# Optimization experiments

Hardware: AMD Instinct MI355X
Metric: run time of the kernel (lower is better)

The kernel has to match this reference:

```python
import jax, jax.numpy as jnp
import numpy as np

N, E = 50000, 1600000
F_IN, EDGE_DIM, HID, HEADS, NCLS = 64, 16, 128, 4, 40
C = HID // HEADS  # per-head dim = 32


def setup_inputs() -> dict:
    key = jax.random.key(0)
    ks = jax.random.split(key, 20)
    s = 0.1
    inp = {
        'x': jax.random.normal(ks[0], (N, F_IN), jnp.float32),
        'edge_index': jax.random.randint(ks[1], (2, E), 0, N, jnp.int64),
        'edge_attr': jax.random.normal(ks[2], (E, EDGE_DIM), jnp.float32),
        # layer 1 params
        'W1': jax.random.normal(ks[3], (HID, F_IN), jnp.float32) * s,
        'as1': jax.random.normal(ks[4], (HEADS, C), jnp.float32) * s,
        'ad1': jax.random.normal(ks[5], (HEADS, C), jnp.float32) * s,
        'ae1': jax.random.normal(ks[6], (HEADS, C), jnp.float32) * s,
        'We1': jax.random.normal(ks[7], (HID, EDGE_DIM), jnp.float32) * s,
        'b1': jnp.zeros((HID,), jnp.float32),
        # layer 2 params
        'W2': jax.random.normal(ks[8], (HID, HID), jnp.float32) * s,
        'as2': jax.random.normal(ks[9], (HEADS, C), jnp.float32) * s,
        'ad2': jax.random.normal(ks[10], (HEADS, C), jnp.float32) * s,
        'ae2': jax.random.normal(ks[11], (HEADS, C), jnp.float32) * s,
        'We2': jax.random.normal(ks[12], (HID, EDGE_DIM), jnp.float32) * s,
        'b2': jnp.zeros((HID,), jnp.float32),
        # final classifier
        'Wlin': jax.random.normal(ks[13], (NCLS, HID), jnp.float32) * s,
        'blin': jnp.zeros((NCLS,), jnp.float32),
    }
    return inp


def gat_conv(x, src, dst, eattr, W, a_s, a_d, a_e, We, b):
    """PyG GATConv (concat=True, add_self_loops=True, fill_value='mean'), eval mode."""
    n = x.shape[0]
    H, Cd = a_s.shape
    h = (x @ W.T).reshape(n, H, Cd)  # [N,H,C]
    # self-loop edge_attr = per-destination mean of incoming edge_attr
    cnt = jax.ops.segment_sum(jnp.ones((dst.shape[0],), eattr.dtype), dst, num_segments=n)
    mean_ea = jax.ops.segment_sum(eattr, dst, num_segments=n) / jnp.maximum(cnt, 1.0)[:, None]
    loops = jnp.arange(n, dtype=src.dtype)
    s_idx = jnp.concatenate([src, loops])
    d_idx = jnp.concatenate([dst, loops])
    ea = jnp.concatenate([eattr, mean_ea], axis=0)  # [E+N, edge_dim]
    e = (ea @ We.T).reshape(-1, H, Cd)
    # edge-wise attention logits
    alpha = (h * a_s).sum(-1)[s_idx] + (h * a_d).sum(-1)[d_idx] + (e * a_e).sum(-1)  # [E+N,H]
    alpha = jax.nn.leaky_relu(alpha, 0.2)
    # segment softmax over destination neighborhoods (every node has a self-loop)
    amax = jax.ops.segment_max(alpha, d_idx, num_segments=n)
    ex = jnp.exp(alpha - amax[d_idx])
    den = jax.ops.segment_sum(ex, d_idx, num_segments=n)
    coef = ex / (den[d_idx] + 1e-16)
    out = jax.ops.segment_sum(h[s_idx] * coef[:, :, None], d_idx, num_segments=n)
    return out.reshape(n, H * Cd) + b


def reference(x, edge_index, edge_attr, W1, as1, ad1, ae1, We1, b1,
              W2, as2, ad2, ae2, We2, b2, Wlin, blin):
    src, dst = edge_index[0], edge_index[1]
    h = jax.nn.relu(gat_conv(x, src, dst, edge_attr, W1, as1, ad1, ae1, We1, b1))
    h = jax.nn.relu(gat_conv(h, src, dst, edge_attr, W2, as2, ad2, ae2, We2, b2))
    logits = h @ Wlin.T + blin
    return jax.nn.log_softmax(logits, axis=1)
```

## Files before the change

kernel.cpp:

```cpp
#include <hip/hip_runtime.h>
#include <hip/hip_bf16.h>
#include <math.h>


#define CHUNK 2048

typedef __attribute__((ext_vector_type(8))) short short8;
typedef __attribute__((ext_vector_type(4))) float floatx4;

__device__ __forceinline__ unsigned short f2bf(float f) {
  unsigned u = __float_as_uint(f);
  unsigned r = u + 0x7FFFu + ((u >> 16) & 1u);
  return (unsigned short)(r >> 16);
}
__device__ __forceinline__ float bf2f(unsigned short b) {
  return __uint_as_float(((unsigned)b) << 16);
}

__global__ __launch_bounds__(128) void wa_kernel(const float* __restrict__ ae1,
                                                 const float* __restrict__ We1,
                                                 const float* __restrict__ ae2,
                                                 const float* __restrict__ We2,
                                                 float* __restrict__ Wa) {
  int t = threadIdx.x;
  const float* ae = (t < 64) ? ae1 : ae2;
  const float* We = (t < 64) ? We1 : We2;
  int h = (t >> 4) & 3;
  int d = t & 15;
  float s = 0.f;
  for (int c = 0; c < 32; ++c) s += ae[h * 32 + c] * We[(h * 32 + c) * 16 + d];
  Wa[t] = s;
}

__global__ __launch_bounds__(256) void alphaseq_kernel(const float* __restrict__ ea,
                                                       const float* __restrict__ Wa,
                                                       uint2* __restrict__ tA1,
                                                       uint2* __restrict__ tA2, int E) {
  __shared__ float wa[128];
  if (threadIdx.x < 128) wa[threadIdx.x] = Wa[threadIdx.x];
  __syncthreads();
  int e = blockIdx.x * 256 + threadIdx.x;
  if (e >= E) return;
  const float4* p = (const float4*)(ea + (size_t)e * 16);
  float4 q0 = p[0], q1 = p[1], q2 = p[2], q3 = p[3];
  float v[16] = {q0.x, q0.y, q0.z, q0.w, q1.x, q1.y, q1.z, q1.w,
                 q2.x, q2.y, q2.z, q2.w, q3.x, q3.y, q3.z, q3.w};
  unsigned short rr[8];
#pragma unroll
  for (int h = 0; h < 8; ++h) {
    float s = 0.f;
#pragma unroll
    for (int d = 0; d < 16; ++d) s += v[d] * wa[h * 16 + d];
    rr[h] = f2bf(s);
  }
  uint2 lo, hi;
  lo.x = ((unsigned)rr[1] << 16) | rr[0];
  lo.y = ((unsigned)rr[3] << 16) | rr[2];
  hi.x = ((unsigned)rr[5] << 16) | rr[4];
  hi.y = ((unsigned)rr[7] << 16) | rr[6];
  tA1[e] = lo;
  tA2[e] = hi;
}

__global__ __launch_bounds__(512) void hist_kernel(const int* __restrict__ dst,
                                                   int* __restrict__ bucketCnt,
                                                   int E, int NB) {
  __shared__ int hist[512];
  const int tid = threadIdx.x;
  hist[tid] = 0;
  __syncthreads();
  const int e0 = blockIdx.x * CHUNK, e1 = min(e0 + CHUNK, E);
  for (int e = e0 + tid; e < e1; e += 512) atomicAdd(&hist[dst[e] >> 7], 1);
  __syncthreads();
  if (tid < NB && hist[tid]) atomicAdd(&bucketCnt[tid], hist[tid]);
}

__global__ __launch_bounds__(512) void scanB_kernel(const int* __restrict__ bucketCnt,
                                                    int* __restrict__ bucketOffs,
                                                    int* __restrict__ bucketPos,
                                                    int* __restrict__ offs,
                                                    int NB, int N, int E) {
  __shared__ int sc[512];
  const int tid = threadIdx.x;
  const int v = (tid < NB) ? bucketCnt[tid] : 0;
  sc[tid] = v;
  __syncthreads();
  for (int off = 1; off < 512; off <<= 1) {
    int t = (tid >= off) ? sc[tid - off] : 0;
    __syncthreads();
    sc[tid] += t;
    __syncthreads();
  }
  const int excl = sc[tid] - v;
  if (tid < NB) { bucketOffs[tid] = excl; bucketPos[tid] = excl; }
  if (tid == 0) { bucketOffs[NB] = E; offs[N] = E; }
}

__global__ __launch_bounds__(512) void partB_kernel(const int* __restrict__ src,
                                                    const int* __restrict__ dst,
                                                    const uint2* __restrict__ tA1,
                                                    const uint2* __restrict__ tA2,
                                                    int* __restrict__ bucketPos,
                                                    int4* __restrict__ binned16,
                                                    int* __restrict__ binned4,
                                                    int E, int NB) {
  __shared__ int hist[512], sc[512], lbase[513], gbase[512], lcnt[512];
  __shared__ int4 stg16[CHUNK];
  __shared__ int stg4[CHUNK];
  const int tid = threadIdx.x;
  const int e0 = blockIdx.x * CHUNK;
  const int e1 = min(e0 + CHUNK, E);
  hist[tid] = 0; lcnt[tid] = 0;
  __syncthreads();
  for (int e = e0 + tid; e < e1; e += 512) atomicAdd(&hist[dst[e] >> 7], 1);
  __syncthreads();
  sc[tid] = hist[tid];
  __syncthreads();
  for (int off = 1; off < 512; off <<= 1) {
    int t = (tid >= off) ? sc[tid - off] : 0;
    __syncthreads();
    sc[tid] += t;
    __syncthreads();
  }
  lbase[tid + 1] = sc[tid];
  if (tid == 0) lbase[0] = 0;
  if (tid < NB && hist[tid] > 0) gbase[tid] = atomicAdd(&bucketPos[tid], hist[tid]);
  __syncthreads();
  for (int e = e0 + tid; e < e1; e += 512) {
    const int d = dst[e];
    const int b = d >> 7;
    const int lr = atomicAdd(&lcnt[b], 1);
    const uint2 a1 = tA1[e];
    const uint2 a2 = tA2[e];
    int4 v;
    v.x = (src[e] & 0xFFFF) | ((d & 127) << 16);
    v.y = (int)a1.x;
    v.z = (int)a1.y;
    v.w = (int)a2.x;
    const int sp = lbase[b] + lr;
    stg16[sp] = v;
    stg4[sp] = (int)a2.y;
  }
  __syncthreads();
  const int total = e1 - e0;
  for (int t = tid; t < total; t += 512) {
    int lo = 0, hi = 511;
    while (lo < hi) {
      int mid = (lo + hi + 1) >> 1;
      if (lbase[mid] <= t) lo = mid; else hi = mid - 1;
    }
    const int g = gbase[lo] + (t - lbase[lo]);
    binned16[g] = stg16[t];
    binned4[g] = stg4[t];
  }
}

__global__ __launch_bounds__(256) void passC_kernel(const int4* __restrict__ binned16,
                                                    const int* __restrict__ binned4,
                                                    const int* __restrict__ bucketOffs,
                                                    int* __restrict__ srcS,
                                                    uint2* __restrict__ aeS1,
                                                    uint2* __restrict__ aeS2,
                                                    int* __restrict__ offs, int N) {
  __shared__ int cnt[128], dbase[129], dpos[128];
  const int tid = threadIdx.x;
  const int b = blockIdx.x;
  const int bo = bucketOffs[b], be = bucketOffs[b + 1];
  const int m = be - bo;
  if (tid < 128) { cnt[tid] = 0; dpos[tid] = 0; }
  __syncthreads();
  for (int t = tid; t < m; t += 256) {
    const int4 v = binned16[bo + t];
    atomicAdd(&cnt[(v.x >> 16) & 127], 1);
  }
  __syncthreads();
  for (int off = 1; off < 128; off <<= 1) {
    int t = (tid < 128 && tid >= (unsigned)off) ? cnt[tid - off] : 0;
    __syncthreads();
    if (tid < 128) cnt[tid] += t;
    __syncthreads();
  }
  if (tid == 0) dbase[0] = 0;
  if (tid < 128) dbase[tid + 1] = cnt[tid];
  __syncthreads();
  const int dcnt = min(128, N - (b << 7));
  if (tid < dcnt) offs[(b << 7) + tid] = bo + dbase[tid];
  for (int t = tid; t < m; t += 256) {
    const int4 v = binned16[bo + t];
    const int w4 = binned4[bo + t];
    const int dl = (v.x >> 16) & 127;
    const int p = dbase[dl] + atomicAdd(&dpos[dl], 1);
    srcS[bo + p] = v.x & 0xFFFF;
    aeS1[bo + p] = make_uint2((unsigned)v.y, (unsigned)v.z);
    aeS2[bo + p] = make_uint2((unsigned)v.w, (unsigned)w4);
  }
}

__global__ __launch_bounds__(256) void cvt3_kernel(const float* __restrict__ a,
                                                   unsigned short* __restrict__ ao, int na,
                                                   const float* __restrict__ b,
                                                   unsigned short* __restrict__ bo, int nb,
                                                   const float* __restrict__ c,
                                                   unsigned short* __restrict__ co, int nc) {
  int i = blockIdx.x * 256 + threadIdx.x;
  if (i < na) ao[i] = f2bf(a[i]);
  else if (i < na + nb) bo[i - na] = f2bf(b[i - na]);
  else if (i < na + nb + nc) co[i - na - nb] = f2bf(c[i - na - nb]);
}

__global__ __launch_bounds__(256) void cvtw_kernel(const float* __restrict__ Wlin,
                                                   unsigned short* __restrict__ whi,
                                                   unsigned short* __restrict__ wlo) {
  int i = blockIdx.x * 256 + threadIdx.x;
  if (i >= 48 * 128) return;
  float v = (i < 40 * 128) ? Wlin[i] : 0.f;
  unsigned short h = f2bf(v);
  whi[i] = h;
  wlo[i] = f2bf(v - bf2f(h));
}

__global__ __launch_bounds__(256) void gemm_mfma_kernel(const unsigned short* __restrict__ X,
                                                        const unsigned short* __restrict__ Wb,
                                                        unsigned short* __restrict__ H,
                                                        int n, int K) {
  const int w = threadIdx.x >> 6;
  const int lane = threadIdx.x & 63;
  const int m0 = blockIdx.x * 64;
  const int quad = lane >> 4;
  const int l15 = lane & 15;
  floatx4 acc[4][2];
#pragma unroll
  for (int mt = 0; mt < 4; ++mt)
#pragma unroll
    for (int nt = 0; nt < 2; ++nt) acc[mt][nt] = (floatx4)(0.f);

  int rowm[4];
#pragma unroll
  for (int mt = 0; mt < 4; ++mt) {
    int r = m0 + mt * 16 + l15;
    rowm[mt] = (r < n) ? r : (n - 1);
  }
  const int ncol0 = (w << 5) + l15;

  for (int kc = 0; kc < K; kc += 32) {
    const int koff = kc + (quad << 3);
    short8 a[4], b[2];
#pragma unroll
    for (int mt = 0; mt < 4; ++mt)
      a[mt] = *(const short8*)(X + (size_t)rowm[mt] * K + koff);
#pragma unroll
    for (int nt = 0; nt < 2; ++nt)
      b[nt] = *(const short8*)(Wb + (size_t)(ncol0 + nt * 16) * K + koff);
#pragma unroll
    for (int mt = 0; mt < 4; ++mt)
#pragma unroll
      for (int nt = 0; nt < 2; ++nt)
        acc[mt][nt] = __builtin_amdgcn_mfma_f32_16x16x32_bf16(a[mt], b[nt], acc[mt][nt], 0, 0, 0);
  }
#pragma unroll
  for (int mt = 0; mt < 4; ++mt) {
    const int rbase = m0 + mt * 16 + (quad << 2);
#pragma unroll
    for (int nt = 0; nt < 2; ++nt) {
      const int col = ncol0 + nt * 16;
#pragma unroll
      for (int r = 0; r < 4; ++r) {
        const int row = rbase + r;
        if (row < n) H[(size_t)row * 128 + col] = f2bf(acc[mt][nt][r]);
      }
    }
  }
}

__global__ __launch_bounds__(256) void score_kernel(const unsigned short* __restrict__ h,
                                                    const float* __restrict__ a_s,
                                                    const float* __restrict__ a_d,
                                                    float* __restrict__ ssc,
                                                    float* __restrict__ dsc, int n) {
  int gid = blockIdx.x * 256 + threadIdx.x;
  int node = gid >> 6;
  int lane = threadIdx.x & 63;
  if (node >= n) return;
  int ch = lane * 2;
  ushort2 hq = *(const ushort2*)(h + (size_t)node * 128 + ch);
  float h0 = bf2f(hq.x), h1 = bf2f(hq.y);
  float ps = h0 * a_s[ch] + h1 * a_s[ch + 1];
  float pd = h0 * a_d[ch] + h1 * a_d[ch + 1];
#pragma unroll
  for (int off = 8; off; off >>= 1) {
    ps += __shfl_xor(ps, off, 16);
    pd += __shfl_xor(pd, off, 16);
  }
  if ((lane & 15) == 0) {
    int head = lane >> 4;
    ssc[node * 4 + head] = ps;
    dsc[node * 4 + head] = pd;
  }
}

__device__ __forceinline__ float leaky02(float a) { return a > 0.f ? a : 0.2f * a; }
__device__ __forceinline__ float sel4(float4 v, int h) {
  return (h == 0) ? v.x : (h == 1) ? v.y : (h == 2) ? v.z : v.w;
}

__global__ __launch_bounds__(256) void agg_kernel(const unsigned short* __restrict__ hin,
                                                  const float* __restrict__ ssc,
                                                  const float* __restrict__ dsc,
                                                  const unsigned short* __restrict__ aeS,
                                                  const int* __restrict__ offs,
                                                  const int* __restrict__ srcS,
                                                  const float* __restrict__ bias,
                                                  unsigned short* __restrict__ hout, int n) {
  __shared__ int sbuf[4][64];
  __shared__ float pbuf[4][256];
  const int tid = threadIdx.x;
  const int wv = tid >> 6;
  const int lane = tid & 63;
  const int node = blockIdx.x * 4 + wv;
  if (node >= n) return;
  const int l32 = lane & 31;
  const int half = lane >> 5;
  const int ch4 = l32 * 4;
  const int headB = l32 >> 3;
  const float4 dv = *(const float4*)(dsc + (size_t)node * 4);
  float4 l4 = make_float4(0.f, 0.f, 0.f, 0.f);
  float4 sa = make_float4(0.f, 0.f, 0.f, 0.f);
  float acc[4] = {0.f, 0.f, 0.f, 0.f};
  const int j0 = offs[node], j1 = offs[node + 1];

  for (int jc = j0; jc < j1; jc += 64) {
    const int len = min(64, j1 - jc);
    float4 p4 = make_float4(0.f, 0.f, 0.f, 0.f);
    int sv = 0;
    if (lane < len) {
      const int j = jc + lane;
      sv = srcS[j];
      const ushort4 aq = *(const ushort4*)(aeS + (size_t)j * 4);
      const float4 ae4 = make_float4(bf2f(aq.x), bf2f(aq.y), bf2f(aq.z), bf2f(aq.w));
      const float4 ss4 = *(const float4*)(ssc + (size_t)sv * 4);
      sa.x += ae4.x; sa.y += ae4.y; sa.z += ae4.z; sa.w += ae4.w;
      p4.x = __expf(leaky02(ss4.x + dv.x + ae4.x));
      p4.y = __expf(leaky02(ss4.y + dv.y + ae4.y));
      p4.z = __expf(leaky02(ss4.z + dv.z + ae4.z));
      p4.w = __expf(leaky02(ss4.w + dv.w + ae4.w));
    }
    sbuf[wv][lane] = sv;
    *(float4*)(&pbuf[wv][lane * 4]) = p4;
    l4.x += p4.x; l4.y += p4.y; l4.z += p4.z; l4.w += p4.w;
    int k = 0;
    for (; k + 8 <= len; k += 8) {
      int kk0 = k + half, kk1 = k + 2 + half, kk2 = k + 4 + half, kk3 = k + 6 + half;
      int s0 = sbuf[wv][kk0], s1 = sbuf[wv][kk1], s2 = sbuf[wv][kk2], s3 = sbuf[wv][kk3];
      float p0 = pbuf[wv][kk0 * 4 + headB], p1 = pbuf[wv][kk1 * 4 + headB];
      float p2 = pbuf[wv][kk2 * 4 + headB], p3 = pbuf[wv][kk3 * 4 + headB];
      uint2 d0 = *(const uint2*)(hin + (size_t)s0 * 128 + ch4);
      uint2 d1 = *(const uint2*)(hin + (size_t)s1 * 128 + ch4);
      uint2 d2 = *(const uint2*)(hin + (size_t)s2 * 128 + ch4);
      uint2 d3 = *(const uint2*)(hin + (size_t)s3 * 128 + ch4);
      acc[0] += p0 * __uint_as_float(d0.x << 16);
      acc[1] += p0 * __uint_as_float(d0.x & 0xFFFF0000u);
      acc[2] += p0 * __uint_as_float(d0.y << 16);
      acc[3] += p0 * __uint_as_float(d0.y & 0xFFFF0000u);
      acc[0] += p1 * __uint_as_float(d1.x << 16);
      acc[1] += p1 * __uint_as_float(d1.x & 0xFFFF0000u);
      acc[2] += p1 * __uint_as_float(d1.y << 16);
      acc[3] += p1 * __uint_as_float(d1.y & 0xFFFF0000u);
      acc[0] += p2 * __uint_as_float(d2.x << 16);
      acc[1] += p2 * __uint_as_float(d2.x & 0xFFFF0000u);
      acc[2] += p2 * __uint_as_float(d2.y << 16);
      acc[3] += p2 * __uint_as_float(d2.y & 0xFFFF0000u);
      acc[0] += p3 * __uint_as_float(d3.x << 16);
      acc[1] += p3 * __uint_as_float(d3.x & 0xFFFF0000u);
      acc[2] += p3 * __uint_as_float(d3.y << 16);
      acc[3] += p3 * __uint_as_float(d3.y & 0xFFFF0000u);
    }
    for (; k < len; k += 2) {
      int kk = k + half;
      if (kk < len) {
        int s = sbuf[wv][kk];
        float p = pbuf[wv][kk * 4 + headB];
        uint2 d = *(const uint2*)(hin + (size_t)s * 128 + ch4);
        acc[0] += p * __uint_as_float(d.x << 16);
        acc[1] += p * __uint_as_float(d.x & 0xFFFF0000u);
        acc[2] += p * __uint_as_float(d.y << 16);
        acc[3] += p * __uint_as_float(d.y & 0xFFFF0000u);
      }
    }
  }

#pragma unroll
  for (int off = 32; off; off >>= 1) {
    sa.x += __shfl_xor(sa.x, off);
    sa.y += __shfl_xor(sa.y, off);
    sa.z += __shfl_xor(sa.z, off);
    sa.w += __shfl_xor(sa.w, off);
    l4.x += __shfl_xor(l4.x, off);
    l4.y += __shfl_xor(l4.y, off);
    l4.z += __shfl_xor(l4.z, off);
    l4.w += __shfl_xor(l4.w, off);
  }
#pragma unroll
  for (int i = 0; i < 4; ++i) acc[i] += __shfl_xor(acc[i], 32);

  const int deg = j1 - j0;
  const float invd = 1.f / fmaxf((float)deg, 1.f);
  const float ssn = ssc[(size_t)node * 4 + headB];
  const float aloop = leaky02(ssn + sel4(dv, headB) + sel4(sa, headB) * invd);
  const float pl = __expf(aloop);
  const float lF = sel4(l4, headB) + pl;
  const uint2 hd = *(const uint2*)(hin + (size_t)node * 128 + ch4);
  const float hv0 = __uint_as_float(hd.x << 16);
  const float hv1 = __uint_as_float(hd.x & 0xFFFF0000u);
  const float hv2 = __uint_as_float(hd.y << 16);
  const float hv3 = __uint_as_float(hd.y & 0xFFFF0000u);
  const float inv = 1.f / (lF + 1e-16f);
  const float4 bi = *(const float4*)(bias + ch4);
  const float o0 = fmaxf((acc[0] + pl * hv0) * inv + bi.x, 0.f);
  const float o1 = fmaxf((acc[1] + pl * hv1) * inv + bi.y, 0.f);
  const float o2 = fmaxf((acc[2] + pl * hv2) * inv + bi.z, 0.f);
  const float o3 = fmaxf((acc[3] + pl * hv3) * inv + bi.w, 0.f);
  if (half == 0) {
    ushort4 o;
    o.x = f2bf(o0); o.y = f2bf(o1); o.z = f2bf(o2); o.w = f2bf(o3);
    *(ushort4*)(hout + (size_t)node * 128 + ch4) = o;
  }
}

__global__ __launch_bounds__(256) void classifier_kernel(const unsigned short* __restrict__ h,
                                                         const unsigned short* __restrict__ Whi,
                                                         const unsigned short* __restrict__ Wlo,
                                                         const float* __restrict__ blin,
                                                         float* __restrict__ out, int n) {
  const int w = threadIdx.x >> 6;
  const int lane = threadIdx.x & 63;
  const int quad = lane >> 4;
  const int l15 = lane & 15;
  const int row0 = blockIdx.x * 64 + w * 16;
  if (row0 >= n) return;
  int rowm = row0 + l15;
  if (rowm >= n) rowm = n - 1;
  floatx4 acc[3];
#pragma unroll
  for (int nt = 0; nt < 3; ++nt) acc[nt] = (floatx4)(0.f);
  const size_t hbase = (size_t)rowm * 128;
#pragma unroll
  for (int kc = 0; kc < 128; kc += 32) {
    const int koff = kc + (quad << 3);
    short8 a = *(const short8*)(h + hbase + koff);
#pragma unroll
    for (int nt = 0; nt < 3; ++nt) {
      short8 bh = *(const short8*)(Whi + (size_t)(nt * 16 + l15) * 128 + koff);
      short8 bl = *(const short8*)(Wlo + (size_t)(nt * 16 + l15) * 128 + koff);
      acc[nt] = __builtin_amdgcn_mfma_f32_16x16x32_bf16(a, bh, acc[nt], 0, 0, 0);
      acc[nt] = __builtin_amdgcn_mfma_f32_16x16x32_bf16(a, bl, acc[nt], 0, 0, 0);
    }
  }
  const float bl0 = blin[l15];
  const float bl1 = blin[16 + l15];
  const float bl2 = (l15 < 8) ? blin[32 + l15] : 0.f;
#pragma unroll
  for (int r = 0; r < 4; ++r) {
    const int rrow = row0 + (quad << 2) + r;
    const float v0 = acc[0][r] + bl0;
    const float v1 = acc[1][r] + bl1;
    const float v2 = (l15 < 8) ? (acc[2][r] + bl2) : -INFINITY;
    float m = fmaxf(v0, fmaxf(v1, v2));
#pragma unroll
    for (int off = 8; off; off >>= 1) m = fmaxf(m, __shfl_xor(m, off, 16));
    const float e2 = (l15 < 8) ? __expf(v2 - m) : 0.f;
    float s = __expf(v0 - m) + __expf(v1 - m) + e2;
#pragma unroll
    for (int off = 8; off; off >>= 1) s += __shfl_xor(s, off, 16);
    const float ls = m + __logf(s);
    if (rrow < n) {
      float* po = out + (size_t)rrow * 40;
      po[l15] = v0 - ls;
      po[16 + l15] = v1 - ls;
      if (l15 < 8) po[32 + l15] = v2 - ls;
    }
  }
}

extern "C" void kernel_launch(void* const* d_in, const int* in_sizes, int n_in,
                              void* d_out, int out_size, void* d_ws, size_t ws_size,
                              hipStream_t stream) {
  const float* x    = (const float*)d_in[0];
  const int*   eidx = (const int*)d_in[1];
  const float* ea   = (const float*)d_in[2];
  const float* W1   = (const float*)d_in[3];
  const float* as1  = (const float*)d_in[4];
  const float* ad1  = (const float*)d_in[5];
  const float* ae1w = (const float*)d_in[6];
  const float* We1  = (const float*)d_in[7];
  const float* b1   = (const float*)d_in[8];
  const float* W2   = (const float*)d_in[9];
  const float* as2  = (const float*)d_in[10];
  const float* ad2  = (const float*)d_in[11];
  const float* ae2w = (const float*)d_in[12];
  const float* We2  = (const float*)d_in[13];
  const float* b2   = (const float*)d_in[14];
  const float* Wlin = (const float*)d_in[15];
  const float* blin = (const float*)d_in[16];
  float* out = (float*)d_out;

  const int N = in_sizes[0] / 64;
  const int E = in_sizes[1] / 2;
  const int* src = eidx;
  const int* dst = eidx + E;
  const int NB = (N + 127) >> 7;

  char* wsb = (char*)d_ws;
  size_t off = 0;
  auto alloc = [&](size_t bytes) -> void* {
    void* p = wsb + off;
    off = (off + bytes + 255) & ~(size_t)255;
    return p;
  };
  int* bucketCnt  = (int*)alloc(512 * 4);
  int* bucketOffs = (int*)alloc(513 * 4);
  int* bucketPos  = (int*)alloc(512 * 4);
  int* offs       = (int*)alloc((size_t)(N + 1) * 4);
  uint2* tA1      = (uint2*)alloc((size_t)E * 8);
  uint2* tA2      = (uint2*)alloc((size_t)E * 8);
  void* regC      = alloc((size_t)E * 16);
  int4* binned16  = (int4*)regC;
  unsigned short* hA = (unsigned short*)regC;
  void* regD      = alloc((size_t)E * 4);
  int* binned4    = (int*)regD;
  unsigned short* xb = (unsigned short*)regD;
  int* srcS       = (int*)alloc((size_t)E * 4);
  float* Wa       = (float*)alloc(128 * 4);
  unsigned short* Wb1 = (unsigned short*)alloc(128 * 64 * 2);
  unsigned short* Wb2 = (unsigned short*)alloc(128 * 128 * 2);
  unsigned short* Wlh = (unsigned short*)alloc(48 * 128 * 2);
  unsigned short* Wll = (unsigned short*)alloc(48 * 128 * 2);
  float* ssc      = (float*)alloc((size_t)N * 4 * 4);
  float* dsc      = (float*)alloc((size_t)N * 4 * 4);
  unsigned short* hB = (unsigned short*)alloc((size_t)N * 128 * 2);
  uint2* aeS1 = tA1;
  uint2* aeS2 = tA2;

  const int ge = (E + 255) / 256;
  const int gg = (N + 63) / 64;
  const int gs = (N + 3) / 4;
  const int gp = (E + CHUNK - 1) / CHUNK;
  const int ncvt = N * 64 + 128 * 64 + 128 * 128;

  hipMemsetAsync(bucketCnt, 0, 512 * 4, stream);
  wa_kernel<<<1, 128, 0, stream>>>(ae1w, We1, ae2w, We2, Wa);
  alphaseq_kernel<<<ge, 256, 0, stream>>>(ea, Wa, tA1, tA2, E);
  hist_kernel<<<gp, 512, 0, stream>>>(dst, bucketCnt, E, NB);
  scanB_kernel<<<1, 512, 0, stream>>>(bucketCnt, bucketOffs, bucketPos, offs, NB, N, E);
  partB_kernel<<<gp, 512, 0, stream>>>(src, dst, tA1, tA2, bucketPos, binned16, binned4, E, NB);
  passC_kernel<<<NB, 256, 0, stream>>>(binned16, binned4, bucketOffs, srcS, aeS1, aeS2, offs, N);

  cvt3_kernel<<<(ncvt + 255) / 256, 256, 0, stream>>>(x, xb, N * 64, W1, Wb1, 128 * 64,
                                                      W2, Wb2, 128 * 128);
  cvtw_kernel<<<24, 256, 0, stream>>>(Wlin, Wlh, Wll);

  gemm_mfma_kernel<<<gg, 256, 0, stream>>>(xb, Wb1, hA, N, 64);
  score_kernel<<<gs, 256, 0, stream>>>(hA, as1, ad1, ssc, dsc, N);
  agg_kernel<<<gs, 256, 0, stream>>>(hA, ssc, dsc, (const unsigned short*)aeS1, offs, srcS, b1, hB, N);

  gemm_mfma_kernel<<<gg, 256, 0, stream>>>(hB, Wb2, hA, N, 128);
  score_kernel<<<gs, 256, 0, stream>>>(hA, as2, ad2, ssc, dsc, N);
  agg_kernel<<<gs, 256, 0, stream>>>(hA, ssc, dsc, (const unsigned short*)aeS2, offs, srcS, b2, hB, N);

  classifier_kernel<<<gg, 256, 0, stream>>>(hB, Wlh, Wll, blin, out, N);
}
```

Baseline: 490.6 us.

## Fuse x bf16 conversion into first GEMM, add byte dest-local array, pack agg FMAs

The first-layer GEMM now reads fp32 x directly and converts to bf16 in registers. This removes the separate conversion pass over N*64 elements and its intermediate buffer. partB also writes a one-byte destination-local index per edge, so passC's histogram pass reads 1 byte instead of 16 per edge, at the cost of an extra write. The aggregation inner loop is restructured to use float2 vector accumulators, which may map to packed FMA instructions.

```diff
diff --git a/kernel.cpp b/kernel.cpp
--- a/kernel.cpp
+++ b/kernel.cpp
@@ -7,6 +7,7 @@
 
 typedef __attribute__((ext_vector_type(8))) short short8;
 typedef __attribute__((ext_vector_type(4))) float floatx4;
+typedef __attribute__((ext_vector_type(2))) float floatx2;
 
 __device__ __forceinline__ unsigned short f2bf(float f) {
   unsigned u = __float_as_uint(f);
@@ -103,10 +104,12 @@
                                                     int* __restrict__ bucketPos,
                                                     int4* __restrict__ binned16,
                                                     int* __restrict__ binned4,
+                                                    unsigned char* __restrict__ dlArr,
                                                     int E, int NB) {
   __shared__ int hist[512], sc[512], lbase[513], gbase[512], lcnt[512];
   __shared__ int4 stg16[CHUNK];
   __shared__ int stg4[CHUNK];
+  __shared__ unsigned char stg1[CHUNK];
   const int tid = threadIdx.x;
   const int e0 = blockIdx.x * CHUNK;
   const int e1 = min(e0 + CHUNK, E);
@@ -140,6 +143,7 @@
     const int sp = lbase[b] + lr;
     stg16[sp] = v;
     stg4[sp] = (int)a2.y;
+    stg1[sp] = (unsigned char)(d & 127);
   }
   __syncthreads();
   const int total = e1 - e0;
@@ -152,11 +156,13 @@
     const int g = gbase[lo] + (t - lbase[lo]);
     binned16[g] = stg16[t];
     binned4[g] = stg4[t];
+    dlArr[g] = stg1[t];
   }
 }
 
 __global__ __launch_bounds__(256) void passC_kernel(const int4* __restrict__ binned16,
                                                     const int* __restrict__ binned4,
+                                                    const unsigned char* __restrict__ dlArr,
                                                     const int* __restrict__ bucketOffs,
                                                     int* __restrict__ srcS,
                                                     uint2* __restrict__ aeS1,
@@ -169,10 +175,7 @@
   const int m = be - bo;
   if (tid < 128) { cnt[tid] = 0; dpos[tid] = 0; }
   __syncthreads();
-  for (int t = tid; t < m; t += 256) {
-    const int4 v = binned16[bo + t];
-    atomicAdd(&cnt[(v.x >> 16) & 127], 1);
-  }
+  for (int t = tid; t < m; t += 256) atomicAdd(&cnt[dlArr[bo + t]], 1);
   __syncthreads();
   for (int off = 1; off < 128; off <<= 1) {
     int t = (tid < 128 && tid >= (unsigned)off) ? cnt[tid - off] : 0;
@@ -196,16 +199,13 @@
   }
 }
 
-__global__ __launch_bounds__(256) void cvt3_kernel(const float* __restrict__ a,
+__global__ __launch_bounds__(256) void cvt2_kernel(const float* __restrict__ a,
                                                    unsigned short* __restrict__ ao, int na,
                                                    const float* __restrict__ b,
-                                                   unsigned short* __restrict__ bo, int nb,
-                                                   const float* __restrict__ c,
-                                                   unsigned short* __restrict__ co, int nc) {
+                                                   unsigned short* __restrict__ bo, int nb) {
   int i = blockIdx.x * 256 + threadIdx.x;
   if (i < na) ao[i] = f2bf(a[i]);
   else if (i < na + nb) bo[i - na] = f2bf(b[i - na]);
-  else if (i < na + nb + nc) co[i - na - nb] = f2bf(c[i - na - nb]);
 }
 
 __global__ __launch_bounds__(256) void cvtw_kernel(const float* __restrict__ Wlin,
@@ -217,6 +217,67 @@
   unsigned short h = f2bf(v);
   whi[i] = h;
   wlo[i] = f2bf(v - bf2f(h));
+}
+
+__global__ __launch_bounds__(256) void gemm_mfma_f32_kernel(const float* __restrict__ X,
+                                                            const unsigned short* __restrict__ Wb,
+                                                            unsigned short* __restrict__ H,
+                                                            int n) {
+  const int w = threadIdx.x >> 6;
+  const int lane = threadIdx.x & 63;
+  const int m0 = blockIdx.x * 64;
+  const int quad = lane >> 4;
+  const int l15 = lane & 15;
+  floatx4 acc[4][2];
+#pragma unroll
+  for (int mt = 0; mt < 4; ++mt)
+#pragma unroll
+    for (int nt = 0; nt < 2; ++nt) acc[mt][nt] = (floatx4)(0.f);
+
+  int rowm[4];
+#pragma unroll
+  for (int mt = 0; mt < 4; ++mt) {
+    int r = m0 + mt * 16 + l15;
+    rowm[mt] = (r < n) ? r : (n - 1);
+  }
+  const int ncol0 = (w << 5) + l15;
+
+#pragma unroll
+  for (int kc = 0; kc < 64; kc += 32) {
+    const int koff = kc + (quad << 3);
+    short8 a[4], b[2];
+#pragma unroll
+    for (int mt = 0; mt < 4; ++mt) {
+      const float* pr = X + (size_t)rowm[mt] * 64 + koff;
+      float4 q0 = *(const float4*)pr;
+      float4 q1 = *(const float4*)(pr + 4);
+      a[mt][0] = (short)f2bf(q0.x); a[mt][1] = (short)f2bf(q0.y);
+      a[mt][2] = (short)f2bf(q0.z); a[mt][3] = (short)f2bf(q0.w);
+      a[mt][4] = (short)f2bf(q1.x); a[mt][5] = (short)f2bf(q1.y);
+      a[mt][6] = (short)f2bf(q1.z); a[mt][7] = (short)f2bf(q1.w);
+    }
+#pragma unroll
+    for (int nt = 0; nt < 2; ++nt)
+      b[nt] = *(const short8*)(Wb + (size_t)(ncol0 + nt * 16) * 64 + koff);
+#pragma unroll
+    for (int mt = 0; mt < 4; ++mt)
+#pragma unroll
+      for (int nt = 0; nt < 2; ++nt)
+        acc[mt][nt] = __builtin_amdgcn_mfma_f32_16x16x32_bf16(a[mt], b[nt], acc[mt][nt], 0, 0, 0);
+  }
+#pragma unroll
+  for (int mt = 0; mt < 4; ++mt) {
+    const int rbase = m0 + mt * 16 + (quad << 2);
+#pragma unroll
+    for (int nt = 0; nt < 2; ++nt) {
+      const int col = ncol0 + nt * 16;
+#pragma unroll
+      for (int r = 0; r < 4; ++r) {
+        const int row = rbase + r;
+        if (row < n) H[(size_t)row * 128 + col] = f2bf(acc[mt][nt][r]);
+      }
+    }
+  }
 }
 
 __global__ __launch_bounds__(256) void gemm_mfma_kernel(const unsigned short* __restrict__ X,
@@ -325,7 +386,8 @@
   const float4 dv = *(const float4*)(dsc + (size_t)node * 4);
   float4 l4 = make_float4(0.f, 0.f, 0.f, 0.f);
   float4 sa = make_float4(0.f, 0.f, 0.f, 0.f);
-  float acc[4] = {0.f, 0.f, 0.f, 0.f};
+  floatx2 acc01 = (floatx2)(0.f);
+  floatx2 acc23 = (floatx2)(0.f);
   const int j0 = offs[node], j1 = offs[node + 1];
 
   for (int jc = j0; jc < j1; jc += 64) {
@@ -349,30 +411,29 @@
     l4.x += p4.x; l4.y += p4.y; l4.z += p4.z; l4.w += p4.w;
     int k = 0;
     for (; k + 8 <= len; k += 8) {
-      int kk0 = k + half, kk1 = k + 2 + half, kk2 = k + 4 + half, kk3 = k + 6 + half;
-      int s0 = sbuf[wv][kk0], s1 = sbuf[wv][kk1], s2 = sbuf[wv][kk2], s3 = sbuf[wv][kk3];
-      float p0 = pbuf[wv][kk0 * 4 + headB], p1 = pbuf[wv][kk1 * 4 + headB];
-      float p2 = pbuf[wv][kk2 * 4 + headB], p3 = pbuf[wv][kk3 * 4 + headB];
-      uint2 d0 = *(const uint2*)(hin + (size_t)s0 * 128 + ch4);
-      uint2 d1 = *(const uint2*)(hin + (size_t)s1 * 128 + ch4);
-      uint2 d2 = *(const uint2*)(hin + (size_t)s2 * 128 + ch4);
-      uint2 d3 = *(const uint2*)(hin + (size_t)s3 * 128 + ch4);
-      acc[0] += p0 * __uint_as_float(d0.x << 16);
-      acc[1] += p0 * __uint_as_float(d0.x & 0xFFFF0000u);
-      acc[2] += p0 * __uint_as_float(d0.y << 16);
-      acc[3] += p0 * __uint_as_float(d0.y & 0xFFFF0000u);
-      acc[0] += p1 * __uint_as_float(d1.x << 16);
-      acc[1] += p1 * __uint_as_float(d1.x & 0xFFFF0000u);
-      acc[2] += p1 * __uint_as_float(d1.y << 16);
-      acc[3] += p1 * __uint_as_float(d1.y & 0xFFFF0000u);
-      acc[0] += p2 * __uint_as_float(d2.x << 16);
-      acc[1] += p2 * __uint_as_float(d2.x & 0xFFFF0000u);
-      acc[2] += p2 * __uint_as_float(d2.y << 16);
-      acc[3] += p2 * __uint_as_float(d2.y & 0xFFFF0000u);
-      acc[0] += p3 * __uint_as_float(d3.x << 16);
-      acc[1] += p3 * __uint_as_float(d3.x & 0xFFFF0000u);
-      acc[2] += p3 * __uint_as_float(d3.y << 16);
-      acc[3] += p3 * __uint_as_float(d3.y & 0xFFFF0000u);
+      int s[4];
+      float p[4];
+      uint2 d[4];
+#pragma unroll
+      for (int u = 0; u < 4; ++u) {
+        const int kk = k + 2 * u + half;
+        s[u] = sbuf[wv][kk];
+        p[u] = pbuf[wv][kk * 4 + headB];
+      }
+#pragma unroll
+      for (int u = 0; u < 4; ++u)
+        d[u] = *(const uint2*)(hin + (size_t)s[u] * 128 + ch4);
+#pragma unroll
+      for (int u = 0; u < 4; ++u) {
+        floatx2 p2; p2.x = p[u]; p2.y = p[u];
+        floatx2 h01, h23;
+        h01.x = __uint_as_float(d[u].x << 16);
+        h01.y = __uint_as_float(d[u].x & 0xFFFF0000u);
+        h23.x = __uint_as_float(d[u].y << 16);
+        h23.y = __uint_as_float(d[u].y & 0xFFFF0000u);
+        acc01 += p2 * h01;
+        acc23 += p2 * h23;
+      }
     }
     for (; k < len; k += 2) {
       int kk = k + half;
@@ -380,14 +441,19 @@
         int s = sbuf[wv][kk];
         float p = pbuf[wv][kk * 4 + headB];
         uint2 d = *(const uint2*)(hin + (size_t)s * 128 + ch4);
-        acc[0] += p * __uint_as_float(d.x << 16);
-        acc[1] += p * __uint_as_float(d.x & 0xFFFF0000u);
-        acc[2] += p * __uint_as_float(d.y << 16);
-        acc[3] += p * __uint_as_float(d.y & 0xFFFF0000u);
+        floatx2 p2; p2.x = p; p2.y = p;
+        floatx2 h01, h23;
+        h01.x = __uint_as_float(d.x << 16);
+        h01.y = __uint_as_float(d.x & 0xFFFF0000u);
+        h23.x = __uint_as_float(d.y << 16);
+        h23.y = __uint_as_float(d.y & 0xFFFF0000u);
+        acc01 += p2 * h01;
+        acc23 += p2 * h23;
       }
     }
   }
 
+  float acc[4] = {acc01.x, acc01.y, acc23.x, acc23.y};
 #pragma unroll
   for (int off = 32; off; off >>= 1) {
     sa.x += __shfl_xor(sa.x, off);
@@ -525,9 +591,8 @@
   void* regC      = alloc((size_t)E * 16);
   int4* binned16  = (int4*)regC;
   unsigned short* hA = (unsigned short*)regC;
-  void* regD      = alloc((size_t)E * 4);
-  int* binned4    = (int*)regD;
-  unsigned short* xb = (unsigned short*)regD;
+  int* binned4    = (int*)alloc((size_t)E * 4);
+  unsigned char* dlArr = (unsigned char*)alloc((size_t)E);
   int* srcS       = (int*)alloc((size_t)E * 4);
   float* Wa       = (float*)alloc(128 * 4);
   unsigned short* Wb1 = (unsigned short*)alloc(128 * 64 * 2);
@@ -544,21 +609,22 @@
   const int gg = (N + 63) / 64;
   const int gs = (N + 3) / 4;
   const int gp = (E + CHUNK - 1) / CHUNK;
-  const int ncvt = N * 64 + 128 * 64 + 128 * 128;
+  const int ncvt = 128 * 64 + 128 * 128;
 
   hipMemsetAsync(bucketCnt, 0, 512 * 4, stream);
   wa_kernel<<<1, 128, 0, stream>>>(ae1w, We1, ae2w, We2, Wa);
   alphaseq_kernel<<<ge, 256, 0, stream>>>(ea, Wa, tA1, tA2, E);
   hist_kernel<<<gp, 512, 0, stream>>>(dst, bucketCnt, E, NB);
   scanB_kernel<<<1, 512, 0, stream>>>(bucketCnt, bucketOffs, bucketPos, offs, NB, N, E);
-  partB_kernel<<<gp, 512, 0, stream>>>(src, dst, tA1, tA2, bucketPos, binned16, binned4, E, NB);
-  passC_kernel<<<NB, 256, 0, stream>>>(binned16, binned4, bucketOffs, srcS, aeS1, aeS2, offs, N);
-
-  cvt3_kernel<<<(ncvt + 255) / 256, 256, 0, stream>>>(x, xb, N * 64, W1, Wb1, 128 * 64,
-                                                      W2, Wb2, 128 * 128);
+  partB_kernel<<<gp, 512, 0, stream>>>(src, dst, tA1, tA2, bucketPos, binned16, binned4,
+                                       dlArr, E, NB);
+  passC_kernel<<<NB, 256, 0, stream>>>(binned16, binned4, dlArr, bucketOffs, srcS,
+                                       aeS1, aeS2, offs, N);
+
+  cvt2_kernel<<<(ncvt + 255) / 256, 256, 0, stream>>>(W1, Wb1, 128 * 64, W2, Wb2, 128 * 128);
   cvtw_kernel<<<24, 256, 0, stream>>>(Wlin, Wlh, Wll);
 
-  gemm_mfma_kernel<<<gg, 256, 0, stream>>>(xb, Wb1, hA, N, 64);
+  gemm_mfma_f32_kernel<<<gg, 256, 0, stream>>>(x, Wb1, hA, N);
   score_kernel<<<gs, 256, 0, stream>>>(hA, as1, ad1, ssc, dsc, N);
   agg_kernel<<<gs, 256, 0, stream>>>(hA, ssc, dsc, (const unsigned short*)aeS1, offs, srcS, b1, hB, N);
 
```

After: 488.2 us. About the same (-0.5%).
